# Optimization experiments

Hardware: AMD Instinct MI355X
Metric: run time of the kernel (lower is better)

Reference implementation:

```python
import jax, jax.numpy as jnp
import numpy as np

B, S, H, D = 4, 2048, 16, 64
CAUSAL = True
NEG_INF = -1e30


def setup_inputs() -> dict:
    key = jax.random.key(0)
    k1, k2, k3, k4 = jax.random.split(key, 4)
    q = jax.random.normal(k1, (B, S, H, D), dtype=jnp.float32)
    k = jax.random.normal(k2, (B, S, H, D), dtype=jnp.float32)
    v = jax.random.normal(k3, (B, S, H, D), dtype=jnp.float32)
    bias = jax.random.normal(k4, (1, H, S, S), dtype=jnp.float32)
    return {"q": q, "k": k, "v": v, "bias": bias}


def reference(q, k, v, bias):
    # q,k,v: [B, S, H, D]; bias: [1, H, S, S] (broadcast over batch)
    scale = 1.0 / jnp.sqrt(jnp.asarray(D, dtype=q.dtype))
    # scores: [B, H, Sq, Sk]
    s = jnp.einsum('bqhd,bkhd->bhqk', q, k) * scale + bias
    if CAUSAL:
        causal_mask = jnp.tril(jnp.ones((S, S), dtype=bool))  # [Sq, Sk]
        s = jnp.where(causal_mask[None, None, :, :], s, NEG_INF)
    p = jax.nn.softmax(s, axis=-1)
    out = jnp.einsum('bhqk,bkhd->bqhd', p, v)  # [B, S, H, D]
    return out
```

## Files before the change

kernel.cpp:

```cpp
#include <hip/hip_runtime.h>

typedef __attribute__((ext_vector_type(8))) short short8;
typedef __attribute__((ext_vector_type(4))) float floatx4;

constexpr int kS = 2048, kH = 16, kD = 64;
constexpr int kBatch = 4;
constexpr float kScale = 0.125f;
constexpr int LSTR = 72;

__device__ inline unsigned short f2bf(float x) {
  unsigned u = __float_as_uint(x);
  u += 0x7fffu + ((u >> 16) & 1u);
  return (unsigned short)(u >> 16);
}

__global__ __launch_bounds__(256) void prepass_kernel(
    const float* __restrict__ Q, const float* __restrict__ K,
    const float* __restrict__ V, unsigned short* __restrict__ Qb,
    unsigned short* __restrict__ Kb, unsigned short* __restrict__ Vt) {
  __shared__ unsigned short vs[64 * LSTR];
  const int t = threadIdx.x;
  const int st = blockIdx.x, h = blockIdx.y, b = blockIdx.z;
  const int bh = b * kH + h;
  const int r = t >> 2, c = (t & 3) * 16;
  const int s = st * 64 + r;
  const size_t in_off = ((size_t)(b * kS + s) * kH + h) * kD + c;
  const size_t qk_out = ((size_t)bh * kS + s) * kD + c;

  unsigned short tmp[16];
  {
    const float4* ip = (const float4*)(Q + in_off);
#pragma unroll
    for (int i = 0; i < 4; ++i) {
      float4 f = ip[i];
      tmp[i*4+0]=f2bf(f.x); tmp[i*4+1]=f2bf(f.y); tmp[i*4+2]=f2bf(f.z); tmp[i*4+3]=f2bf(f.w);
    }
    *(uint4*)(Qb + qk_out) = *(const uint4*)&tmp[0];
    *(uint4*)(Qb + qk_out + 8) = *(const uint4*)&tmp[8];
  }
  {
    const float4* ip = (const float4*)(K + in_off);
#pragma unroll
    for (int i = 0; i < 4; ++i) {
      float4 f = ip[i];
      tmp[i*4+0]=f2bf(f.x); tmp[i*4+1]=f2bf(f.y); tmp[i*4+2]=f2bf(f.z); tmp[i*4+3]=f2bf(f.w);
    }
    *(uint4*)(Kb + qk_out) = *(const uint4*)&tmp[0];
    *(uint4*)(Kb + qk_out + 8) = *(const uint4*)&tmp[8];
  }
  {
    const float4* ip = (const float4*)(V + in_off);
#pragma unroll
    for (int i = 0; i < 4; ++i) {
      float4 f = ip[i];
      tmp[i*4+0]=f2bf(f.x); tmp[i*4+1]=f2bf(f.y); tmp[i*4+2]=f2bf(f.z); tmp[i*4+3]=f2bf(f.w);
    }
    *(uint4*)&vs[r * LSTR + c] = *(const uint4*)&tmp[0];
    *(uint4*)&vs[r * LSTR + c + 8] = *(const uint4*)&tmp[8];
  }
  __syncthreads();
  unsigned short tv[16];
#pragma unroll
  for (int i = 0; i < 16; ++i) tv[i] = vs[(c + i) * LSTR + r];
  const size_t vt_out = ((size_t)bh * kD + r) * kS + st * 64 + c;
  *(uint4*)(Vt + vt_out) = *(const uint4*)&tv[0];
  *(uint4*)(Vt + vt_out + 8) = *(const uint4*)&tv[8];
}

__global__ __launch_bounds__(256, 4) void fa_mfma_kernel(
    const unsigned short* __restrict__ Qb, const unsigned short* __restrict__ Kb,
    const unsigned short* __restrict__ Vt, const float* __restrict__ Bias,
    float* __restrict__ O) {
  __shared__ unsigned short Ks[64 * LSTR];
  __shared__ unsigned short Vs[64 * LSTR];
  __shared__ unsigned short QPs[64 * LSTR];

  const int t = threadIdx.x;
  const int lane = t & 63, w = t >> 6;
  const int quad = lane >> 4, l16 = lane & 15;

  const int idx = blockIdx.x;
  const int b = idx & 3;
  const int h = (idx >> 2) & 15;
  const int qt = 31 - (idx >> 6);
  const int bh = b * kH + h;

  const int sr = t >> 2, sc = (t & 3) * 16;

  {
    const uint4* src = (const uint4*)(Qb + ((size_t)bh * kS + qt * 64 + sr) * kD + sc);
    uint4* dst = (uint4*)&QPs[sr * LSTR + sc];
    dst[0] = src[0]; dst[1] = src[1];
  }
  unsigned short* Psw = QPs + w * 16 * LSTR;

  short8 aQ[2];
  aQ[0] = *(const short8*)&Psw[l16 * LSTR + quad * 8];
  aQ[1] = *(const short8*)&Psw[l16 * LSTR + quad * 8 + 32];

  floatx4 acc[4];
  float lp[4];
#pragma unroll
  for (int i = 0; i < 4; ++i) {
    acc[i] = (floatx4){0.f, 0.f, 0.f, 0.f};
    lp[i] = 0.f;
  }

  const int qrow_base = qt * 64 + w * 16 + quad * 4;
  const float* bpr[4];
#pragma unroll
  for (int reg = 0; reg < 4; ++reg)
    bpr[reg] = Bias + (size_t)h * kS * kS + (size_t)(qrow_base + reg) * kS + l16;

  uint4 kr0, kr1, vr0, vr1;
  {
    const uint4* srck = (const uint4*)(Kb + ((size_t)bh * kS + sr) * kD + sc);
    kr0 = srck[0]; kr1 = srck[1];
    const uint4* srcv = (const uint4*)(Vt + ((size_t)bh * kD + sr) * kS + sc);
    vr0 = srcv[0]; vr1 = srcv[1];
  }
  float bb[4][4];
#pragma unroll
  for (int reg = 0; reg < 4; ++reg)
#pragma unroll
    for (int nt = 0; nt < 4; ++nt) bb[reg][nt] = bpr[reg][nt * 16];

  for (int kb = 0; kb <= qt; ++kb) {
    const int k0 = kb * 64;
    __syncthreads();
    *(uint4*)&Ks[sr * LSTR + sc] = kr0;
    *(uint4*)&Ks[sr * LSTR + sc + 8] = kr1;
    *(uint4*)&Vs[sr * LSTR + sc] = vr0;
    *(uint4*)&Vs[sr * LSTR + sc + 8] = vr1;
    __syncthreads();

    if (kb < qt) {
      const uint4* srck = (const uint4*)(Kb + ((size_t)bh * kS + k0 + 64 + sr) * kD + sc);
      kr0 = srck[0]; kr1 = srck[1];
      const uint4* srcv = (const uint4*)(Vt + ((size_t)bh * kD + sr) * kS + k0 + 64 + sc);
      vr0 = srcv[0]; vr1 = srcv[1];
    }

    const bool diag = (kb == qt);
    float p[4][4];
#pragma unroll
    for (int nt = 0; nt < 4; ++nt) {
      short8 b0 = *(const short8*)&Ks[(nt * 16 + l16) * LSTR + quad * 8];
      short8 b1 = *(const short8*)&Ks[(nt * 16 + l16) * LSTR + quad * 8 + 32];
      floatx4 cf = (floatx4){0.f, 0.f, 0.f, 0.f};
      cf = __builtin_amdgcn_mfma_f32_16x16x32_bf16(aQ[0], b0, cf, 0, 0, 0);
      cf = __builtin_amdgcn_mfma_f32_16x16x32_bf16(aQ[1], b1, cf, 0, 0, 0);
      const int col = k0 + nt * 16 + l16;
#pragma unroll
      for (int reg = 0; reg < 4; ++reg) {
        const float x = cf[reg] * kScale + bb[reg][nt];
        p[reg][nt] = (diag && col > qrow_base + reg) ? 0.f : __expf(x);
      }
    }

    if (kb < qt) {
#pragma unroll
      for (int reg = 0; reg < 4; ++reg)
#pragma unroll
        for (int nt = 0; nt < 4; ++nt)
          bb[reg][nt] = bpr[reg][(size_t)(k0 + 64 + nt * 16)];
    }

#pragma unroll
    for (int reg = 0; reg < 4; ++reg) {
      lp[reg] += (p[reg][0] + p[reg][1]) + (p[reg][2] + p[reg][3]);
#pragma unroll
      for (int nt = 0; nt < 4; ++nt)
        Psw[(quad * 4 + reg) * LSTR + nt * 16 + l16] = f2bf(p[reg][nt]);
    }

#pragma unroll
    for (int ks = 0; ks < 2; ++ks) {
      short8 aP = *(const short8*)&Psw[l16 * LSTR + ks * 32 + quad * 8];
#pragma unroll
      for (int dt = 0; dt < 4; ++dt) {
        short8 bV = *(const short8*)&Vs[(dt * 16 + l16) * LSTR + ks * 32 + quad * 8];
        acc[dt] = __builtin_amdgcn_mfma_f32_16x16x32_bf16(aP, bV, acc[dt], 0, 0, 0);
      }
    }
  }

#pragma unroll
  for (int reg = 0; reg < 4; ++reg) {
    float l = lp[reg];
    l += __shfl_xor(l, 1, 64);
    l += __shfl_xor(l, 2, 64);
    l += __shfl_xor(l, 4, 64);
    l += __shfl_xor(l, 8, 64);
    const float inv_l = 1.f / l;
    float* op = O + ((size_t)(b * kS + qrow_base + reg) * kH + h) * kD;
#pragma unroll
    for (int dt = 0; dt < 4; ++dt)
      op[dt * 16 + l16] = acc[dt][reg] * inv_l;
  }
}

extern "C" void kernel_launch(void* const* d_in, const int* in_sizes, int n_in,
                              void* d_out, int out_size, void* d_ws, size_t ws_size,
                              hipStream_t stream) {
  const float* q = (const float*)d_in[0];
  const float* k = (const float*)d_in[1];
  const float* v = (const float*)d_in[2];
  const float* bias = (const float*)d_in[3];
  float* out = (float*)d_out;

  const size_t elems = (size_t)kBatch * kH * kS * kD;
  unsigned short* Qb = (unsigned short*)d_ws;
  unsigned short* Kb = Qb + elems;
  unsigned short* Vt = Kb + elems;

  dim3 pgrid(kS / 64, kH, kBatch);
  prepass_kernel<<<pgrid, dim3(256), 0, stream>>>(q, k, v, Qb, Kb, Vt);
  fa_mfma_kernel<<<dim3(32 * kH * kBatch), dim3(256), 0, stream>>>(Qb, Kb, Vt, bias, out);
}
```

Baseline: 502.8 us.

## Double-buffer K/V in LDS, transpose QK^T MFMA for vectorized bias loads

K and V tiles now go into two LDS buffers, so the next tile is stored while the current one is consumed, leaving one barrier per iteration instead of two. The QK^T MFMA operands are swapped so each lane holds four consecutive key columns of a single query row. This lets the bias be read as float4 vectors, and the row-sum reduction shrinks to two shuffles. Q is loaded straight from global memory into registers, and P is packed with the v_cvt_pk_bf16_f32 instruction. Occupancy drops to 3 blocks per CU because LDS use and register pressure go up.

Result: no change. 494.7 us (-1.6%).

```diff
diff --git a/kernel.cpp b/kernel.cpp
--- a/kernel.cpp
+++ b/kernel.cpp
@@ -12,6 +12,12 @@
   unsigned u = __float_as_uint(x);
   u += 0x7fffu + ((u >> 16) & 1u);
   return (unsigned short)(u >> 16);
+}
+
+__device__ inline unsigned cvt_pk_bf16(float lo, float hi) {
+  unsigned r;
+  asm("v_cvt_pk_bf16_f32 %0, %1, %2" : "=v"(r) : "v"(lo), "v"(hi));
+  return r;
 }
 
 __global__ __launch_bounds__(256) void prepass_kernel(
@@ -67,13 +73,13 @@
   *(uint4*)(Vt + vt_out + 8) = *(const uint4*)&tv[8];
 }
 
-__global__ __launch_bounds__(256, 4) void fa_mfma_kernel(
+__global__ __launch_bounds__(256, 3) void fa_mfma_kernel(
     const unsigned short* __restrict__ Qb, const unsigned short* __restrict__ Kb,
     const unsigned short* __restrict__ Vt, const float* __restrict__ Bias,
     float* __restrict__ O) {
-  __shared__ unsigned short Ks[64 * LSTR];
-  __shared__ unsigned short Vs[64 * LSTR];
-  __shared__ unsigned short QPs[64 * LSTR];
+  __shared__ unsigned short Ks[2][64 * LSTR];
+  __shared__ unsigned short Vs[2][64 * LSTR];
+  __shared__ unsigned short Ps[64 * LSTR];
 
   const int t = threadIdx.x;
   const int lane = t & 63, w = t >> 6;
@@ -87,91 +93,77 @@
 
   const int sr = t >> 2, sc = (t & 3) * 16;
 
-  {
-    const uint4* src = (const uint4*)(Qb + ((size_t)bh * kS + qt * 64 + sr) * kD + sc);
-    uint4* dst = (uint4*)&QPs[sr * LSTR + sc];
-    dst[0] = src[0]; dst[1] = src[1];
-  }
-  unsigned short* Psw = QPs + w * 16 * LSTR;
+  const int qrow = qt * 64 + w * 16 + l16;
 
   short8 aQ[2];
-  aQ[0] = *(const short8*)&Psw[l16 * LSTR + quad * 8];
-  aQ[1] = *(const short8*)&Psw[l16 * LSTR + quad * 8 + 32];
+  {
+    const unsigned short* qp = Qb + ((size_t)bh * kS + qrow) * kD + quad * 8;
+    aQ[0] = *(const short8*)qp;
+    aQ[1] = *(const short8*)(qp + 32);
+  }
+
+  unsigned short* Psw = Ps + w * 16 * LSTR;
 
   floatx4 acc[4];
-  float lp[4];
-#pragma unroll
-  for (int i = 0; i < 4; ++i) {
-    acc[i] = (floatx4){0.f, 0.f, 0.f, 0.f};
-    lp[i] = 0.f;
-  }
-
-  const int qrow_base = qt * 64 + w * 16 + quad * 4;
-  const float* bpr[4];
-#pragma unroll
-  for (int reg = 0; reg < 4; ++reg)
-    bpr[reg] = Bias + (size_t)h * kS * kS + (size_t)(qrow_base + reg) * kS + l16;
+#pragma unroll
+  for (int i = 0; i < 4; ++i) acc[i] = (floatx4){0.f, 0.f, 0.f, 0.f};
+  float lp = 0.f;
+
+  const float* bp = Bias + (size_t)h * kS * kS + (size_t)qrow * kS + quad * 4;
+  const unsigned short* Kbh = Kb + (size_t)bh * kS * kD;
+  const unsigned short* Vbh = Vt + (size_t)bh * kD * kS;
 
   uint4 kr0, kr1, vr0, vr1;
-  {
-    const uint4* srck = (const uint4*)(Kb + ((size_t)bh * kS + sr) * kD + sc);
+  float4 bbA[4], bbB[4];
+
+  {
+    const uint4* srck = (const uint4*)(Kbh + (size_t)sr * kD + sc);
     kr0 = srck[0]; kr1 = srck[1];
-    const uint4* srcv = (const uint4*)(Vt + ((size_t)bh * kD + sr) * kS + sc);
+    const uint4* srcv = (const uint4*)(Vbh + (size_t)sr * kS + sc);
     vr0 = srcv[0]; vr1 = srcv[1];
   }
-  float bb[4][4];
-#pragma unroll
-  for (int reg = 0; reg < 4; ++reg)
-#pragma unroll
-    for (int nt = 0; nt < 4; ++nt) bb[reg][nt] = bpr[reg][nt * 16];
-
-  for (int kb = 0; kb <= qt; ++kb) {
+#pragma unroll
+  for (int nt = 0; nt < 4; ++nt) bbA[nt] = *(const float4*)(bp + nt * 16);
+  *(uint4*)&Ks[0][sr * LSTR + sc] = kr0;
+  *(uint4*)&Ks[0][sr * LSTR + sc + 8] = kr1;
+  *(uint4*)&Vs[0][sr * LSTR + sc] = vr0;
+  *(uint4*)&Vs[0][sr * LSTR + sc + 8] = vr1;
+  if (qt > 0) {
+    const uint4* srck = (const uint4*)(Kbh + (size_t)(64 + sr) * kD + sc);
+    kr0 = srck[0]; kr1 = srck[1];
+    const uint4* srcv = (const uint4*)(Vbh + (size_t)sr * kS + 64 + sc);
+    vr0 = srcv[0]; vr1 = srcv[1];
+#pragma unroll
+    for (int nt = 0; nt < 4; ++nt) bbB[nt] = *(const float4*)(bp + 64 + nt * 16);
+  }
+  __syncthreads();
+
+  auto iter = [&](const int kb, const unsigned short* Kc, const unsigned short* Vc,
+                  unsigned short* Kn, unsigned short* Vn, float4* bb) {
     const int k0 = kb * 64;
-    __syncthreads();
-    *(uint4*)&Ks[sr * LSTR + sc] = kr0;
-    *(uint4*)&Ks[sr * LSTR + sc + 8] = kr1;
-    *(uint4*)&Vs[sr * LSTR + sc] = vr0;
-    *(uint4*)&Vs[sr * LSTR + sc + 8] = vr1;
-    __syncthreads();
-
-    if (kb < qt) {
-      const uint4* srck = (const uint4*)(Kb + ((size_t)bh * kS + k0 + 64 + sr) * kD + sc);
-      kr0 = srck[0]; kr1 = srck[1];
-      const uint4* srcv = (const uint4*)(Vt + ((size_t)bh * kD + sr) * kS + k0 + 64 + sc);
-      vr0 = srcv[0]; vr1 = srcv[1];
-    }
-
     const bool diag = (kb == qt);
-    float p[4][4];
+
 #pragma unroll
     for (int nt = 0; nt < 4; ++nt) {
-      short8 b0 = *(const short8*)&Ks[(nt * 16 + l16) * LSTR + quad * 8];
-      short8 b1 = *(const short8*)&Ks[(nt * 16 + l16) * LSTR + quad * 8 + 32];
+      short8 a0 = *(const short8*)&Kc[(nt * 16 + l16) * LSTR + quad * 8];
+      short8 a1 = *(const short8*)&Kc[(nt * 16 + l16) * LSTR + quad * 8 + 32];
       floatx4 cf = (floatx4){0.f, 0.f, 0.f, 0.f};
-      cf = __builtin_amdgcn_mfma_f32_16x16x32_bf16(aQ[0], b0, cf, 0, 0, 0);
-      cf = __builtin_amdgcn_mfma_f32_16x16x32_bf16(aQ[1], b1, cf, 0, 0, 0);
-      const int col = k0 + nt * 16 + l16;
+      cf = __builtin_amdgcn_mfma_f32_16x16x32_bf16(a0, aQ[0], cf, 0, 0, 0);
+      cf = __builtin_amdgcn_mfma_f32_16x16x32_bf16(a1, aQ[1], cf, 0, 0, 0);
+      const int colb = k0 + nt * 16 + quad * 4;
+      const float* bf = (const float*)&bb[nt];
+      float p[4];
 #pragma unroll
       for (int reg = 0; reg < 4; ++reg) {
-        const float x = cf[reg] * kScale + bb[reg][nt];
-        p[reg][nt] = (diag && col > qrow_base + reg) ? 0.f : __expf(x);
+        const float x = cf[reg] * kScale + bf[reg];
+        float pv = __expf(x);
+        if (diag && (colb + reg > qrow)) pv = 0.f;
+        p[reg] = pv;
       }
-    }
-
-    if (kb < qt) {
-#pragma unroll
-      for (int reg = 0; reg < 4; ++reg)
-#pragma unroll
-        for (int nt = 0; nt < 4; ++nt)
-          bb[reg][nt] = bpr[reg][(size_t)(k0 + 64 + nt * 16)];
-    }
-
-#pragma unroll
-    for (int reg = 0; reg < 4; ++reg) {
-      lp[reg] += (p[reg][0] + p[reg][1]) + (p[reg][2] + p[reg][3]);
-#pragma unroll
-      for (int nt = 0; nt < 4; ++nt)
-        Psw[(quad * 4 + reg) * LSTR + nt * 16 + l16] = f2bf(p[reg][nt]);
+      lp += (p[0] + p[1]) + (p[2] + p[3]);
+      const unsigned u0 = cvt_pk_bf16(p[0], p[1]);
+      const unsigned u1 = cvt_pk_bf16(p[2], p[3]);
+      *(uint2*)&Psw[l16 * LSTR + nt * 16 + quad * 4] = make_uint2(u0, u1);
     }
 
 #pragma unroll
@@ -179,24 +171,44 @@
       short8 aP = *(const short8*)&Psw[l16 * LSTR + ks * 32 + quad * 8];
 #pragma unroll
       for (int dt = 0; dt < 4; ++dt) {
-        short8 bV = *(const short8*)&Vs[(dt * 16 + l16) * LSTR + ks * 32 + quad * 8];
+        short8 bV = *(const short8*)&Vc[(dt * 16 + l16) * LSTR + ks * 32 + quad * 8];
         acc[dt] = __builtin_amdgcn_mfma_f32_16x16x32_bf16(aP, bV, acc[dt], 0, 0, 0);
       }
     }
-  }
-
+
+    if (kb < qt) {
+      *(uint4*)&Kn[sr * LSTR + sc] = kr0;
+      *(uint4*)&Kn[sr * LSTR + sc + 8] = kr1;
+      *(uint4*)&Vn[sr * LSTR + sc] = vr0;
+      *(uint4*)&Vn[sr * LSTR + sc + 8] = vr1;
+      if (kb + 1 < qt) {
+        const int kn = k0 + 128;
+        const uint4* srck = (const uint4*)(Kbh + (size_t)(kn + sr) * kD + sc);
+        kr0 = srck[0]; kr1 = srck[1];
+        const uint4* srcv = (const uint4*)(Vbh + (size_t)sr * kS + kn + sc);
+        vr0 = srcv[0]; vr1 = srcv[1];
+#pragma unroll
+        for (int nt = 0; nt < 4; ++nt) bb[nt] = *(const float4*)(bp + kn + nt * 16);
+      }
+      __syncthreads();
+    }
+  };
+
+  for (int kb = 0; kb <= qt; kb += 2) {
+    iter(kb, Ks[0], Vs[0], Ks[1], Vs[1], bbA);
+    if (kb + 1 <= qt) iter(kb + 1, Ks[1], Vs[1], Ks[0], Vs[0], bbB);
+  }
+
+  lp += __shfl_xor(lp, 16, 64);
+  lp += __shfl_xor(lp, 32, 64);
+  const float linv = 1.f / lp;
 #pragma unroll
   for (int reg = 0; reg < 4; ++reg) {
-    float l = lp[reg];
-    l += __shfl_xor(l, 1, 64);
-    l += __shfl_xor(l, 2, 64);
-    l += __shfl_xor(l, 4, 64);
-    l += __shfl_xor(l, 8, 64);
-    const float inv_l = 1.f / l;
-    float* op = O + ((size_t)(b * kS + qrow_base + reg) * kH + h) * kD;
+    const float il = __shfl(linv, quad * 4 + reg, 16);
+    float* op = O + ((size_t)(b * kS + qt * 64 + w * 16 + quad * 4 + reg) * kH + h) * kD;
 #pragma unroll
     for (int dt = 0; dt < 4; ++dt)
-      op[dt * 16 + l16] = acc[dt][reg] * inv_l;
+      op[dt * 16 + l16] = acc[dt][reg] * il;
   }
 }
 
```
